# Performance work log

Measured on AMD Instinct MI355X. Metric: run time of the kernel, lower is better.

Reference implementation:

```python
import jax, jax.numpy as jnp
import numpy as np

D_MODEL = 1024
D_STATE = 16
D_CONV = 4
EXPAND = 2
DT_RANK = 64  # ceil(d_model / 16)
D_INNER = D_MODEL * EXPAND
BATCH, SEQ_LEN = 2, 2048


def setup_inputs() -> dict:
    key = jax.random.key(0)
    ks = jax.random.split(key, 6)
    s = lambda k, shape, scale: jax.random.normal(k, shape, dtype=jnp.float32) * scale
    x = jax.random.normal(ks[0], (BATCH, SEQ_LEN, D_MODEL), dtype=jnp.float32)
    in_proj_w = s(ks[1], (2 * D_INNER, D_MODEL), D_MODEL ** -0.5)
    conv_w = s(ks[2], (D_INNER, 1, D_CONV), D_CONV ** -0.5)  # depthwise kernel [O, I/groups=1, K]
    conv_b = jnp.zeros((D_INNER,), jnp.float32)
    # HiPPO-inspired init: A_log[d, n] = log(n+1)
    A_log = jnp.log(jnp.broadcast_to(jnp.arange(1, D_STATE + 1, dtype=jnp.float32), (D_INNER, D_STATE)))
    x_proj_w = s(ks[3], (DT_RANK + 2 * D_STATE, D_INNER), D_INNER ** -0.5)
    dt_proj_w = s(ks[4], (D_INNER, DT_RANK), DT_RANK ** -0.5)
    dt_proj_b = jnp.zeros((D_INNER,), jnp.float32)
    D_param = jnp.ones((D_INNER,), jnp.float32)
    out_proj_w = s(ks[5], (D_MODEL, D_INNER), D_INNER ** -0.5)
    return {"x": x, "in_proj_w": in_proj_w, "conv_w": conv_w, "conv_b": conv_b,
            "A_log": A_log, "x_proj_w": x_proj_w, "dt_proj_w": dt_proj_w,
            "dt_proj_b": dt_proj_b, "D": D_param, "out_proj_w": out_proj_w}


def reference(x, in_proj_w, conv_w, conv_b, A_log, x_proj_w, dt_proj_w, dt_proj_b, D, out_proj_w):
    B, L, _ = x.shape
    # input projection -> [B, L, 2*d_inner], split into ssm branch and gate
    xz = x @ in_proj_w.T
    xc, z = jnp.split(xz, 2, axis=-1)
    # depthwise causal conv1d: torch pads (d_conv-1) both sides then truncates -> left pad only
    xt = jnp.transpose(xc, (0, 2, 1))  # [B, d_inner, L]
    xt = jax.lax.conv_general_dilated(
        xt, conv_w, window_strides=(1,), padding=[(D_CONV - 1, 0)],
        dimension_numbers=("NCH", "OIH", "NCH"), feature_group_count=D_INNER)
    xt = xt + conv_b[None, :, None]
    xs = jnp.transpose(xt, (0, 2, 1))  # [B, L, d_inner]
    # input-dependent dt, B, C
    x_dbl = xs @ x_proj_w.T  # [B, L, dt_rank + 2*d_state]
    dt, Bm, Cm = jnp.split(x_dbl, [DT_RANK, DT_RANK + D_STATE], axis=-1)
    dt = jax.nn.softplus(dt @ dt_proj_w.T + dt_proj_b)  # [B, L, d_inner]
    A = -jnp.exp(A_log)  # [d_inner, d_state]

    def step(h, inp):
        x_t, dt_t, B_t, C_t = inp  # [B,d_inner], [B,d_inner], [B,d_state], [B,d_state]
        dA = jnp.exp(dt_t[..., None] * A)                       # [B, d_inner, d_state]
        h = dA * h + (dt_t * x_t)[..., None] * B_t[:, None, :]  # [B, d_inner, d_state]
        y = jnp.einsum("bds,bs->bd", h, C_t)
        return h, y

    h0 = jnp.zeros((B, D_INNER, D_STATE), dtype=x.dtype)
    _, ys = jax.lax.scan(step, h0, (jnp.transpose(xs, (1, 0, 2)),
                                    jnp.transpose(dt, (1, 0, 2)),
                                    jnp.transpose(Bm, (1, 0, 2)),
                                    jnp.transpose(Cm, (1, 0, 2))))
    y = jnp.transpose(ys, (1, 0, 2)) + D * xs          # skip term D * x
    y = y * (z * jax.nn.sigmoid(z))                    # SiLU gate
    return y @ out_proj_w.T
```

## Files before the change

### kernel.cpp

```cpp
#include <hip/hip_runtime.h>
#include <cstdint>
#include <cmath>

#define BATCH   2
#define SEQ     2048
#define DMODEL  1024
#define DINNER  2048
#define DSTATE  16
#define DTRANK  64
#define BL      (BATCH*SEQ)
#define LOG2E   1.44269504088896340736f

typedef __bf16 bf16_t;
typedef bf16_t bf16x4 __attribute__((ext_vector_type(4)));
typedef bf16_t bf16x8 __attribute__((ext_vector_type(8)));
typedef float  f32x4  __attribute__((ext_vector_type(4)));

#define SWZ(r, g) ((g) ^ (((r) >> 1) & 3))

__device__ __forceinline__ void gl16(const bf16_t* g, bf16_t* lds) {
  __builtin_amdgcn_global_load_lds((const __attribute__((address_space(1))) void*)g,
                                   (__attribute__((address_space(3))) void*)lds, 16, 0, 0);
}

__global__ __launch_bounds__(256)
void gemm_hl_mfma(const bf16_t* __restrict__ Ah, const bf16_t* __restrict__ Al,
                  const bf16_t* __restrict__ Wh, const bf16_t* __restrict__ Wl,
                  float* __restrict__ C, int K, int lda, int ldw, int ldc) {
  __shared__ bf16_t smem[2][16384];
  const int m0  = blockIdx.y * 128;
  const int n0  = blockIdx.x * 128;
  const int tid = threadIdx.x;
  const int l   = tid & 63;
  const int w   = tid >> 6;
  const int wr  = w >> 1, wc = w & 1;

  const int r1 = tid >> 2, r2 = (256 + tid) >> 2;
  const int g1 = SWZ(r1, tid & 3), g2 = SWZ(r2, tid & 3);
  const int lb1 = w * 512, lb2 = 2048 + w * 512;
  const int fr = l & 15, kg = l >> 4;

  const size_t kbase = (size_t)blockIdx.z * K;
  C += (size_t)blockIdx.z * (size_t)gridDim.y * 128 * ldc;

  const size_t a1b = (size_t)(m0 + r1) * lda + kbase + g1 * 8;
  const size_t a2b = (size_t)(m0 + r2) * lda + kbase + g2 * 8;
  const size_t w1b = (size_t)(n0 + r1) * ldw + kbase + g1 * 8;
  const size_t w2b = (size_t)(n0 + r2) * ldw + kbase + g2 * 8;

  f32x4 acc[4][4];
#pragma unroll
  for (int i = 0; i < 4; ++i)
#pragma unroll
    for (int j = 0; j < 4; ++j)
      acc[i][j] = (f32x4){0.f, 0.f, 0.f, 0.f};

  const int NT = K >> 5;
  {
    bf16_t* sb = smem[0];
    gl16(Ah + a1b, sb + lb1);         gl16(Ah + a2b, sb + lb2);
    gl16(Al + a1b, sb + 4096 + lb1);  gl16(Al + a2b, sb + 4096 + lb2);
    gl16(Wh + w1b, sb + 8192 + lb1);  gl16(Wh + w2b, sb + 8192 + lb2);
    gl16(Wl + w1b, sb + 12288 + lb1); gl16(Wl + w2b, sb + 12288 + lb2);
  }
  asm volatile("s_waitcnt vmcnt(0)" ::: "memory");
  __syncthreads();

  for (int kt = 0; kt < NT; ++kt) {
    bf16_t* sb = smem[kt & 1];
    if (kt + 1 < NT) {
      bf16_t* sn = smem[(kt + 1) & 1];
      const size_t ko = (size_t)(kt + 1) << 5;
      gl16(Ah + a1b + ko, sn + lb1);         gl16(Ah + a2b + ko, sn + lb2);
      gl16(Al + a1b + ko, sn + 4096 + lb1);  gl16(Al + a2b + ko, sn + 4096 + lb2);
      gl16(Wh + w1b + ko, sn + 8192 + lb1);  gl16(Wh + w2b + ko, sn + 8192 + lb2);
      gl16(Wl + w1b + ko, sn + 12288 + lb1); gl16(Wl + w2b + ko, sn + 12288 + lb2);
    }
    bf16x8 ah[4], al[4], bh[4], bl[4];
#pragma unroll
    for (int mi = 0; mi < 4; ++mi) {
      const int R = wr * 64 + mi * 16 + fr;
      const int e = R * 32 + SWZ(R, kg) * 8;
      ah[mi] = *reinterpret_cast<const bf16x8*>(&sb[e]);
      al[mi] = *reinterpret_cast<const bf16x8*>(&sb[4096 + e]);
    }
#pragma unroll
    for (int ni = 0; ni < 4; ++ni) {
      const int R = wc * 64 + ni * 16 + fr;
      const int e = R * 32 + SWZ(R, kg) * 8;
      bh[ni] = *reinterpret_cast<const bf16x8*>(&sb[8192 + e]);
      bl[ni] = *reinterpret_cast<const bf16x8*>(&sb[12288 + e]);
    }
#pragma unroll
    for (int mi = 0; mi < 4; ++mi)
#pragma unroll
      for (int ni = 0; ni < 4; ++ni) {
        acc[mi][ni] = __builtin_amdgcn_mfma_f32_16x16x32_bf16(ah[mi], bh[ni], acc[mi][ni], 0, 0, 0);
        acc[mi][ni] = __builtin_amdgcn_mfma_f32_16x16x32_bf16(ah[mi], bl[ni], acc[mi][ni], 0, 0, 0);
        acc[mi][ni] = __builtin_amdgcn_mfma_f32_16x16x32_bf16(al[mi], bh[ni], acc[mi][ni], 0, 0, 0);
      }
    if (kt + 1 < NT) asm volatile("s_waitcnt vmcnt(0)" ::: "memory");
    __syncthreads();
  }

#pragma unroll
  for (int mi = 0; mi < 4; ++mi)
#pragma unroll
    for (int i = 0; i < 4; ++i) {
      const int row = m0 + wr * 64 + mi * 16 + (l >> 4) * 4 + i;
#pragma unroll
      for (int ni = 0; ni < 4; ++ni)
        C[(size_t)row * ldc + n0 + wc * 64 + ni * 16 + (l & 15)] = acc[mi][ni][i];
    }
}

__device__ __forceinline__ void cvt4_store(float4 v, bf16_t* hi, bf16_t* lo, int i) {
  bf16x4 h, lv;
  h[0] = (bf16_t)v.x; h[1] = (bf16_t)v.y; h[2] = (bf16_t)v.z; h[3] = (bf16_t)v.w;
  lv[0] = (bf16_t)(v.x - (float)h[0]); lv[1] = (bf16_t)(v.y - (float)h[1]);
  lv[2] = (bf16_t)(v.z - (float)h[2]); lv[3] = (bf16_t)(v.w - (float)h[3]);
  reinterpret_cast<bf16x4*>(hi)[i] = h;
  reinterpret_cast<bf16x4*>(lo)[i] = lv;
}

#define Q1 1048576
#define Q2 (Q1 + 1048576)
#define Q3 (Q2 + 524288)
#define Q4 (Q3 + 32768)
#define Q5 (Q4 + 65536)

__global__ __launch_bounds__(256)
void prep(const float* __restrict__ x, const float* __restrict__ inw,
          const float* __restrict__ outw, const float* __restrict__ dtw,
          const float* __restrict__ xprojw,
          bf16_t* xhi, bf16_t* xlo, bf16_t* iwhi, bf16_t* iwlo,
          bf16_t* owh, bf16_t* owl, bf16_t* dtwh, bf16_t* dtwl,
          bf16_t* xpwh, bf16_t* xpwl) {
  const int i = blockIdx.x * 256 + threadIdx.x;
  if (i < Q1) {
    cvt4_store(reinterpret_cast<const float4*>(x)[i], xhi, xlo, i);
  } else if (i < Q2) {
    const int j = i - Q1;
    cvt4_store(reinterpret_cast<const float4*>(inw)[j], iwhi, iwlo, j);
  } else if (i < Q3) {
    const int j = i - Q2;
    cvt4_store(reinterpret_cast<const float4*>(outw)[j], owh, owl, j);
  } else if (i < Q4) {
    const int j = i - Q3;
    cvt4_store(reinterpret_cast<const float4*>(dtw)[j], dtwh, dtwl, j);
  } else if (i < Q5) {
    const int j = i - Q4;
    const int row = j >> 9;
    float4 v = make_float4(0.f, 0.f, 0.f, 0.f);
    if (row < 96) v = reinterpret_cast<const float4*>(xprojw)[j];
    cvt4_store(v, xpwh, xpwl, j);
  }
}

__global__ __launch_bounds__(256)
void reduce_xdbl(const float* __restrict__ part, float* __restrict__ xdbl,
                 bf16_t* __restrict__ xdh, bf16_t* __restrict__ xdl) {
  const int i = blockIdx.x * 256 + threadIdx.x;
  float4 s = reinterpret_cast<const float4*>(part)[i];
#pragma unroll
  for (int p = 1; p < 8; ++p) {
    const float4 v = reinterpret_cast<const float4*>(part)[(size_t)p * 131072 + i];
    s.x += v.x; s.y += v.y; s.z += v.z; s.w += v.w;
  }
  reinterpret_cast<float4*>(xdbl)[i] = s;
  cvt4_store(s, xdh, xdl, i);
}

__global__ __launch_bounds__(256)
void conv1d_causal_hl(const float* __restrict__ xz, const float* __restrict__ cw,
                      const float* __restrict__ cb, bf16_t* __restrict__ xshi,
                      bf16_t* __restrict__ xslo) {
  const int idx = blockIdx.x * 256 + threadIdx.x;
  const int dq  = idx & 511;
  const int bl  = idx >> 9;
  const int lpos = bl & (SEQ - 1);
  const int d   = dq * 4;

  float wv[4][4];
#pragma unroll
  for (int j = 0; j < 4; ++j)
#pragma unroll
    for (int k = 0; k < 4; ++k)
      wv[j][k] = cw[(size_t)(d + j) * 4 + k];

  float4 acc = *reinterpret_cast<const float4*>(&cb[d]);
#pragma unroll
  for (int k = 0; k < 4; ++k) {
    const int ls = lpos - 3 + k;
    if (ls >= 0) {
      const float4 v = *reinterpret_cast<const float4*>(&xz[(size_t)(bl - 3 + k) * 4096 + d]);
      acc.x += v.x * wv[0][k];
      acc.y += v.y * wv[1][k];
      acc.z += v.z * wv[2][k];
      acc.w += v.w * wv[3][k];
    }
  }
  bf16x4 h, lv;
  h[0] = (bf16_t)acc.x; h[1] = (bf16_t)acc.y; h[2] = (bf16_t)acc.z; h[3] = (bf16_t)acc.w;
  lv[0] = (bf16_t)(acc.x - (float)h[0]); lv[1] = (bf16_t)(acc.y - (float)h[1]);
  lv[2] = (bf16_t)(acc.z - (float)h[2]); lv[3] = (bf16_t)(acc.w - (float)h[3]);
  *reinterpret_cast<bf16x4*>(&xshi[(size_t)bl * 2048 + d]) = h;
  *reinterpret_cast<bf16x4*>(&xslo[(size_t)bl * 2048 + d]) = lv;
}

__device__ __forceinline__ float softplus_f(float v) {
  return fmaxf(v, 0.0f) + log1pf(expf(-fabsf(v)));
}
__device__ __forceinline__ float silu_f(float v) {
  return v / (1.0f + expf(-v));
}

__global__ __launch_bounds__(256)
void scan_pass1(const float* __restrict__ dtg, const bf16_t* __restrict__ xshi,
                const bf16_t* __restrict__ xslo, const float* __restrict__ xdbl,
                const float* __restrict__ alog, const float* __restrict__ dtb,
                float* __restrict__ hP, int NC, int Lc) {
  const int tid = threadIdx.x;
  const int d = blockIdx.x * 256 + tid;
  const int c = blockIdx.y;
  const int b = blockIdx.z;
  __shared__ float sB[64][16];

  float A2[16];
#pragma unroll
  for (int q = 0; q < 4; ++q) {
    const float4 v = *reinterpret_cast<const float4*>(&alog[(size_t)d * 16 + q * 4]);
    A2[q*4+0] = -expf(v.x) * LOG2E; A2[q*4+1] = -expf(v.y) * LOG2E;
    A2[q*4+2] = -expf(v.z) * LOG2E; A2[q*4+3] = -expf(v.w) * LOG2E;
  }
  const float dtbd = dtb[d];

  float h[16];
#pragma unroll
  for (int n = 0; n < 16; ++n) h[n] = 0.f;
  float S = 0.f;

  const int row0c = b * SEQ + c * Lc;
  for (int t0 = 0; t0 < Lc; t0 += 64) {
    const int rows = min(64, Lc - t0);
    __syncthreads();
    for (int j = tid; j < rows * 4; j += 256) {
      const int r = j >> 2, q = j & 3;
      *reinterpret_cast<float4*>(&sB[r][q*4]) =
        *reinterpret_cast<const float4*>(&xdbl[(size_t)(row0c + t0 + r) * 128 + 64 + q*4]);
    }
    __syncthreads();
#pragma unroll 2
    for (int t = 0; t < rows; ++t) {
      const size_t row = (size_t)(row0c + t0 + t);
      const float dtr = dtg[row * 2048 + d];
      const float xv  = (float)xshi[row * 2048 + d] + (float)xslo[row * 2048 + d];
      const float dt  = softplus_f(dtr + dtbd);
      S += dt;
      const float dtx = dt * xv;
#pragma unroll
      for (int n = 0; n < 16; ++n)
        h[n] = fmaf(exp2f(dt * A2[n]), h[n], dtx * sB[t][n]);
    }
  }
  const size_t o = ((((size_t)b * 2048 + d) * NC) + c) * 32;
#pragma unroll
  for (int n = 0; n < 16; ++n) {
    hP[o + n]      = h[n];
    hP[o + 16 + n] = exp2f(A2[n] * S);
  }
}

__global__ __launch_bounds__(256)
void scan_pass2(float* __restrict__ hP, int NC) {
  const int lane = threadIdx.x & 63;
  const int bd   = blockIdx.x * 4 + (threadIdx.x >> 6);
  const int c    = lane < NC ? lane : NC - 1;
  const size_t base = ((size_t)bd * NC + c) * 32;

  float h[16], P[16];
#pragma unroll
  for (int q = 0; q < 4; ++q) {
    const float4 v = *reinterpret_cast<const float4*>(&hP[base + q * 4]);
    h[q*4]=v.x; h[q*4+1]=v.y; h[q*4+2]=v.z; h[q*4+3]=v.w;
    const float4 p = *reinterpret_cast<const float4*>(&hP[base + 16 + q * 4]);
    P[q*4]=p.x; P[q*4+1]=p.y; P[q*4+2]=p.z; P[q*4+3]=p.w;
  }

#pragma unroll
  for (int s = 1; s < 64; s <<= 1) {
    float hf[16], Pf[16];
#pragma unroll
    for (int n = 0; n < 16; ++n) { hf[n] = __shfl_up(h[n], s, 64); Pf[n] = __shfl_up(P[n], s, 64); }
    if (lane >= s) {
#pragma unroll
      for (int n = 0; n < 16; ++n) { h[n] = fmaf(P[n], hf[n], h[n]); P[n] *= Pf[n]; }
    }
  }
  float hx[16];
#pragma unroll
  for (int n = 0; n < 16; ++n) {
    hx[n] = __shfl_up(h[n], 1, 64);
    if (lane == 0) hx[n] = 0.f;
  }
  if (lane < NC) {
#pragma unroll
    for (int q = 0; q < 4; ++q)
      *reinterpret_cast<float4*>(&hP[base + q * 4]) =
        make_float4(hx[q*4], hx[q*4+1], hx[q*4+2], hx[q*4+3]);
  }
}

__global__ __launch_bounds__(256)
void scan_pass3(const float* __restrict__ dtg, const bf16_t* __restrict__ xshi,
                const bf16_t* __restrict__ xslo, const float* __restrict__ xdbl,
                const float* __restrict__ xz, const float* __restrict__ alog,
                const float* __restrict__ dtb, const float* __restrict__ Dp,
                const float* __restrict__ hP, bf16_t* __restrict__ ghi,
                bf16_t* __restrict__ glo, int NC, int Lc) {
  const int tid = threadIdx.x;
  const int d = blockIdx.x * 256 + tid;
  const int c = blockIdx.y;
  const int b = blockIdx.z;
  __shared__ float sB[64][16];
  __shared__ float sC[64][16];

  float A2[16];
#pragma unroll
  for (int q = 0; q < 4; ++q) {
    const float4 v = *reinterpret_cast<const float4*>(&alog[(size_t)d * 16 + q * 4]);
    A2[q*4+0] = -expf(v.x) * LOG2E; A2[q*4+1] = -expf(v.y) * LOG2E;
    A2[q*4+2] = -expf(v.z) * LOG2E; A2[q*4+3] = -expf(v.w) * LOG2E;
  }
  const float dtbd = dtb[d];
  const float Dv   = Dp[d];

  float h[16];
  const size_t o = ((((size_t)b * 2048 + d) * NC) + c) * 32;
#pragma unroll
  for (int q = 0; q < 4; ++q) {
    const float4 v = *reinterpret_cast<const float4*>(&hP[o + q * 4]);
    h[q*4]=v.x; h[q*4+1]=v.y; h[q*4+2]=v.z; h[q*4+3]=v.w;
  }

  const int row0c = b * SEQ + c * Lc;
  for (int t0 = 0; t0 < Lc; t0 += 64) {
    const int rows = min(64, Lc - t0);
    __syncthreads();
    for (int j = tid; j < rows * 8; j += 256) {
      const int r = j >> 3, q = j & 7;
      const float4 v =
        *reinterpret_cast<const float4*>(&xdbl[(size_t)(row0c + t0 + r) * 128 + 64 + q*4]);
      if (q < 4) *reinterpret_cast<float4*>(&sB[r][q*4])     = v;
      else       *reinterpret_cast<float4*>(&sC[r][(q-4)*4]) = v;
    }
    __syncthreads();
#pragma unroll 2
    for (int t = 0; t < rows; ++t) {
      const size_t row = (size_t)(row0c + t0 + t);
      const float dtr = dtg[row * 2048 + d];
      const float xv  = (float)xshi[row * 2048 + d] + (float)xslo[row * 2048 + d];
      const float zv  = xz [row * 4096 + 2048 + d];
      const float dt  = softplus_f(dtr + dtbd);
      const float dtx = dt * xv;
      float ya[4] = {0.f, 0.f, 0.f, 0.f};
#pragma unroll
      for (int n = 0; n < 16; ++n) {
        h[n] = fmaf(exp2f(dt * A2[n]), h[n], dtx * sB[t][n]);
        ya[n & 3] = fmaf(h[n], sC[t][n], ya[n & 3]);
      }
      const float y = (ya[0] + ya[1]) + (ya[2] + ya[3]);
      const float gv = (y + Dv * xv) * silu_f(zv);
      const bf16_t gh = (bf16_t)gv;
      ghi[row * 2048 + d] = gh;
      glo[row * 2048 + d] = (bf16_t)(gv - (float)gh);
    }
  }
}

extern "C" void kernel_launch(void* const* d_in, const int* in_sizes, int n_in,
                              void* d_out, int out_size, void* d_ws, size_t ws_size,
                              hipStream_t stream) {
  const float* x      = (const float*)d_in[0];
  const float* inw    = (const float*)d_in[1];
  const float* convw  = (const float*)d_in[2];
  const float* convb  = (const float*)d_in[3];
  const float* alog   = (const float*)d_in[4];
  const float* xprojw = (const float*)d_in[5];
  const float* dtw    = (const float*)d_in[6];
  const float* dtb    = (const float*)d_in[7];
  const float* Dp     = (const float*)d_in[8];
  const float* outw   = (const float*)d_in[9];
  float* out = (float*)d_out;

  char* p = (char*)d_ws;
  float* xz    = (float*)p;  p += (size_t)BL * 4096 * 4;
  float* xdbl  = (float*)p;  p += (size_t)BL * 128 * 4;
  float* dtg   = (float*)p;  p += (size_t)BL * 2048 * 4;
  bf16_t* xhi  = (bf16_t*)p; p += (size_t)BL * 1024 * 2;
  bf16_t* xlo  = (bf16_t*)p; p += (size_t)BL * 1024 * 2;
  bf16_t* iwhi = (bf16_t*)p; p += (size_t)DINNER*2*1024*2;
  bf16_t* iwlo = (bf16_t*)p; p += (size_t)DINNER*2*1024*2;
  bf16_t* xshi = (bf16_t*)p; p += (size_t)BL * 2048 * 2;
  bf16_t* xslo = (bf16_t*)p; p += (size_t)BL * 2048 * 2;
  bf16_t* xpwh = (bf16_t*)p; p += (size_t)128 * 2048 * 2;
  bf16_t* xpwl = (bf16_t*)p; p += (size_t)128 * 2048 * 2;
  bf16_t* xdh  = (bf16_t*)p; p += (size_t)BL * 128 * 2;
  bf16_t* xdl  = (bf16_t*)p; p += (size_t)BL * 128 * 2;
  bf16_t* dtwh = (bf16_t*)p; p += (size_t)2048 * 64 * 2;
  bf16_t* dtwl = (bf16_t*)p; p += (size_t)2048 * 64 * 2;
  bf16_t* owh  = (bf16_t*)p; p += (size_t)1024 * 2048 * 2;
  bf16_t* owl  = (bf16_t*)p; p += (size_t)1024 * 2048 * 2;
  float* hP    = (float*)p;
  float* xpart = (float*)xhi;
  bf16_t* ghi  = xhi;
  bf16_t* glo  = xhi + (size_t)BL * 2048;

  const size_t base_bytes = (size_t)(p - (char*)d_ws);
  int NC = 64;
  while (NC > 1 && base_bytes + (size_t)BATCH * 2048 * NC * 32 * 4 > ws_size)
    NC >>= 1;
  const int Lc = SEQ / NC;

  prep<<<(Q5 + 255) / 256, 256, 0, stream>>>(x, inw, outw, dtw, xprojw,
      xhi, xlo, iwhi, iwlo, owh, owl, dtwh, dtwl, xpwh, xpwl);
  gemm_hl_mfma<<<dim3(32, 32, 1), 256, 0, stream>>>(xhi, xlo, iwhi, iwlo, xz,
                                                    1024, 1024, 1024, 4096);
  conv1d_causal_hl<<<8192, 256, 0, stream>>>(xz, convw, convb, xshi, xslo);
  gemm_hl_mfma<<<dim3(1, 32, 8), 256, 0, stream>>>(xshi, xslo, xpwh, xpwl, xpart,
                                                   256, 2048, 2048, 128);
  reduce_xdbl<<<512, 256, 0, stream>>>(xpart, xdbl, xdh, xdl);
  gemm_hl_mfma<<<dim3(16, 32, 1), 256, 0, stream>>>(xdh, xdl, dtwh, dtwl, dtg,
                                                    64, 128, 64, 2048);
  scan_pass1<<<dim3(8, NC, 2), 256, 0, stream>>>(dtg, xshi, xslo, xdbl, alog, dtb, hP, NC, Lc);
  scan_pass2<<<1024, 256, 0, stream>>>(hP, NC);
  scan_pass3<<<dim3(8, NC, 2), 256, 0, stream>>>(dtg, xshi, xslo, xdbl, xz, alog, dtb,
                                                 Dp, hP, ghi, glo, NC, Lc);
  gemm_hl_mfma<<<dim3(8, 32, 1), 256, 0, stream>>>(ghi, glo, owh, owl, out,
                                                   2048, 2048, 2048, 1024);
}
```

Before: 517.4 us.

## Fuse softplus and SiLU into GEMM epilogues and use hardware exp2/log2/rcp

Moves the dt softplus (with bias) into the dt-projection GEMM epilogue and the z SiLU into the in-projection GEMM epilogue, so both scan passes read precomputed values. The scan passes stop recomputing softplus twice per element. All exponentials in the scan recurrence now use raw v_exp_f32 instead of exp2f. This removes transcendental work from the serial scan loops, at the cost of slightly lower accuracy from the hardware approximations, and the xz buffer now holds silu(z) rather than z.

```diff
diff --git a/kernel.cpp b/kernel.cpp
--- a/kernel.cpp
+++ b/kernel.cpp
@@ -23,10 +23,22 @@
                                    (__attribute__((address_space(3))) void*)lds, 16, 0, 0);
 }
 
+__device__ __forceinline__ float exp2_hw(float x) { float r; asm("v_exp_f32 %0, %1" : "=v"(r) : "v"(x)); return r; }
+__device__ __forceinline__ float log2_hw(float x) { float r; asm("v_log_f32 %0, %1" : "=v"(r) : "v"(x)); return r; }
+__device__ __forceinline__ float rcp_hw(float x)  { float r; asm("v_rcp_f32 %0, %1" : "=v"(r) : "v"(x)); return r; }
+
+__device__ __forceinline__ float silu_fast(float v) {
+  return v * rcp_hw(1.0f + exp2_hw(-v * LOG2E));
+}
+__device__ __forceinline__ float softplus_fast(float v) {
+  return fmaxf(v, 0.0f) + log2_hw(1.0f + exp2_hw(-fabsf(v) * LOG2E)) * (1.0f / LOG2E);
+}
+
 __global__ __launch_bounds__(256)
 void gemm_hl_mfma(const bf16_t* __restrict__ Ah, const bf16_t* __restrict__ Al,
                   const bf16_t* __restrict__ Wh, const bf16_t* __restrict__ Wl,
-                  float* __restrict__ C, int K, int lda, int ldw, int ldc) {
+                  float* __restrict__ C, int K, int lda, int ldw, int ldc,
+                  const float* __restrict__ bias, int epi) {
   __shared__ bf16_t smem[2][16384];
   const int m0  = blockIdx.y * 128;
   const int n0  = blockIdx.x * 128;
@@ -104,14 +116,22 @@
   }
 
 #pragma unroll
-  for (int mi = 0; mi < 4; ++mi)
-#pragma unroll
-    for (int i = 0; i < 4; ++i) {
-      const int row = m0 + wr * 64 + mi * 16 + (l >> 4) * 4 + i;
-#pragma unroll
-      for (int ni = 0; ni < 4; ++ni)
-        C[(size_t)row * ldc + n0 + wc * 64 + ni * 16 + (l & 15)] = acc[mi][ni][i];
-    }
+  for (int ni = 0; ni < 4; ++ni) {
+    const int col = n0 + wc * 64 + ni * 16 + (l & 15);
+    float bcol = 0.f;
+    if (epi == 1) bcol = bias[col];
+    const bool dosilu = (epi == 2) && (col >= 2048);
+#pragma unroll
+    for (int mi = 0; mi < 4; ++mi)
+#pragma unroll
+      for (int i = 0; i < 4; ++i) {
+        const int row = m0 + wr * 64 + mi * 16 + (l >> 4) * 4 + i;
+        float v = acc[mi][ni][i];
+        if (epi == 1)      v = softplus_fast(v + bcol);
+        else if (dosilu)   v = silu_fast(v);
+        C[(size_t)row * ldc + col] = v;
+      }
+  }
 }
 
 __device__ __forceinline__ void cvt4_store(float4 v, bf16_t* hi, bf16_t* lo, int i) {
@@ -208,18 +228,11 @@
   *reinterpret_cast<bf16x4*>(&xslo[(size_t)bl * 2048 + d]) = lv;
 }
 
-__device__ __forceinline__ float softplus_f(float v) {
-  return fmaxf(v, 0.0f) + log1pf(expf(-fabsf(v)));
-}
-__device__ __forceinline__ float silu_f(float v) {
-  return v / (1.0f + expf(-v));
-}
-
-__global__ __launch_bounds__(256)
-void scan_pass1(const float* __restrict__ dtg, const bf16_t* __restrict__ xshi,
+__global__ __launch_bounds__(256)
+void scan_pass1(const float* __restrict__ dtv, const bf16_t* __restrict__ xshi,
                 const bf16_t* __restrict__ xslo, const float* __restrict__ xdbl,
-                const float* __restrict__ alog, const float* __restrict__ dtb,
-                float* __restrict__ hP, int NC, int Lc) {
+                const float* __restrict__ alog, float* __restrict__ hP,
+                int NC, int Lc) {
   const int tid = threadIdx.x;
   const int d = blockIdx.x * 256 + tid;
   const int c = blockIdx.y;
@@ -230,10 +243,9 @@
 #pragma unroll
   for (int q = 0; q < 4; ++q) {
     const float4 v = *reinterpret_cast<const float4*>(&alog[(size_t)d * 16 + q * 4]);
-    A2[q*4+0] = -expf(v.x) * LOG2E; A2[q*4+1] = -expf(v.y) * LOG2E;
-    A2[q*4+2] = -expf(v.z) * LOG2E; A2[q*4+3] = -expf(v.w) * LOG2E;
-  }
-  const float dtbd = dtb[d];
+    A2[q*4+0] = -exp2_hw(v.x * LOG2E) * LOG2E; A2[q*4+1] = -exp2_hw(v.y * LOG2E) * LOG2E;
+    A2[q*4+2] = -exp2_hw(v.z * LOG2E) * LOG2E; A2[q*4+3] = -exp2_hw(v.w * LOG2E) * LOG2E;
+  }
 
   float h[16];
 #pragma unroll
@@ -253,21 +265,20 @@
 #pragma unroll 2
     for (int t = 0; t < rows; ++t) {
       const size_t row = (size_t)(row0c + t0 + t);
-      const float dtr = dtg[row * 2048 + d];
-      const float xv  = (float)xshi[row * 2048 + d] + (float)xslo[row * 2048 + d];
-      const float dt  = softplus_f(dtr + dtbd);
+      const float dt = dtv[row * 2048 + d];
+      const float xv = (float)xshi[row * 2048 + d] + (float)xslo[row * 2048 + d];
       S += dt;
       const float dtx = dt * xv;
 #pragma unroll
       for (int n = 0; n < 16; ++n)
-        h[n] = fmaf(exp2f(dt * A2[n]), h[n], dtx * sB[t][n]);
+        h[n] = fmaf(exp2_hw(dt * A2[n]), h[n], dtx * sB[t][n]);
     }
   }
   const size_t o = ((((size_t)b * 2048 + d) * NC) + c) * 32;
 #pragma unroll
   for (int n = 0; n < 16; ++n) {
     hP[o + n]      = h[n];
-    hP[o + 16 + n] = exp2f(A2[n] * S);
+    hP[o + 16 + n] = exp2_hw(A2[n] * S);
   }
 }
 
@@ -312,12 +323,12 @@
 }
 
 __global__ __launch_bounds__(256)
-void scan_pass3(const float* __restrict__ dtg, const bf16_t* __restrict__ xshi,
+void scan_pass3(const float* __restrict__ dtv, const bf16_t* __restrict__ xshi,
                 const bf16_t* __restrict__ xslo, const float* __restrict__ xdbl,
                 const float* __restrict__ xz, const float* __restrict__ alog,
-                const float* __restrict__ dtb, const float* __restrict__ Dp,
-                const float* __restrict__ hP, bf16_t* __restrict__ ghi,
-                bf16_t* __restrict__ glo, int NC, int Lc) {
+                const float* __restrict__ Dp, const float* __restrict__ hP,
+                bf16_t* __restrict__ ghi, bf16_t* __restrict__ glo,
+                int NC, int Lc) {
   const int tid = threadIdx.x;
   const int d = blockIdx.x * 256 + tid;
   const int c = blockIdx.y;
@@ -329,11 +340,10 @@
 #pragma unroll
   for (int q = 0; q < 4; ++q) {
     const float4 v = *reinterpret_cast<const float4*>(&alog[(size_t)d * 16 + q * 4]);
-    A2[q*4+0] = -expf(v.x) * LOG2E; A2[q*4+1] = -expf(v.y) * LOG2E;
-    A2[q*4+2] = -expf(v.z) * LOG2E; A2[q*4+3] = -expf(v.w) * LOG2E;
-  }
-  const float dtbd = dtb[d];
-  const float Dv   = Dp[d];
+    A2[q*4+0] = -exp2_hw(v.x * LOG2E) * LOG2E; A2[q*4+1] = -exp2_hw(v.y * LOG2E) * LOG2E;
+    A2[q*4+2] = -exp2_hw(v.z * LOG2E) * LOG2E; A2[q*4+3] = -exp2_hw(v.w * LOG2E) * LOG2E;
+  }
+  const float Dv = Dp[d];
 
   float h[16];
   const size_t o = ((((size_t)b * 2048 + d) * NC) + c) * 32;
@@ -358,19 +368,18 @@
 #pragma unroll 2
     for (int t = 0; t < rows; ++t) {
       const size_t row = (size_t)(row0c + t0 + t);
-      const float dtr = dtg[row * 2048 + d];
-      const float xv  = (float)xshi[row * 2048 + d] + (float)xslo[row * 2048 + d];
-      const float zv  = xz [row * 4096 + 2048 + d];
-      const float dt  = softplus_f(dtr + dtbd);
+      const float dt = dtv[row * 2048 + d];
+      const float xv = (float)xshi[row * 2048 + d] + (float)xslo[row * 2048 + d];
+      const float zs = xz [row * 4096 + 2048 + d];
       const float dtx = dt * xv;
       float ya[4] = {0.f, 0.f, 0.f, 0.f};
 #pragma unroll
       for (int n = 0; n < 16; ++n) {
-        h[n] = fmaf(exp2f(dt * A2[n]), h[n], dtx * sB[t][n]);
+        h[n] = fmaf(exp2_hw(dt * A2[n]), h[n], dtx * sB[t][n]);
         ya[n & 3] = fmaf(h[n], sC[t][n], ya[n & 3]);
       }
       const float y = (ya[0] + ya[1]) + (ya[2] + ya[3]);
-      const float gv = (y + Dv * xv) * silu_f(zv);
+      const float gv = (y + Dv * xv) * zs;
       const bf16_t gh = (bf16_t)gv;
       ghi[row * 2048 + d] = gh;
       glo[row * 2048 + d] = (bf16_t)(gv - (float)gh);
@@ -425,17 +434,17 @@
   prep<<<(Q5 + 255) / 256, 256, 0, stream>>>(x, inw, outw, dtw, xprojw,
       xhi, xlo, iwhi, iwlo, owh, owl, dtwh, dtwl, xpwh, xpwl);
   gemm_hl_mfma<<<dim3(32, 32, 1), 256, 0, stream>>>(xhi, xlo, iwhi, iwlo, xz,
-                                                    1024, 1024, 1024, 4096);
+                                                    1024, 1024, 1024, 4096, nullptr, 2);
   conv1d_causal_hl<<<8192, 256, 0, stream>>>(xz, convw, convb, xshi, xslo);
   gemm_hl_mfma<<<dim3(1, 32, 8), 256, 0, stream>>>(xshi, xslo, xpwh, xpwl, xpart,
-                                                   256, 2048, 2048, 128);
+                                                   256, 2048, 2048, 128, nullptr, 0);
   reduce_xdbl<<<512, 256, 0, stream>>>(xpart, xdbl, xdh, xdl);
   gemm_hl_mfma<<<dim3(16, 32, 1), 256, 0, stream>>>(xdh, xdl, dtwh, dtwl, dtg,
-                                                    64, 128, 64, 2048);
-  scan_pass1<<<dim3(8, NC, 2), 256, 0, stream>>>(dtg, xshi, xslo, xdbl, alog, dtb, hP, NC, Lc);
+                                                    64, 128, 64, 2048, dtb, 1);
+  scan_pass1<<<dim3(8, NC, 2), 256, 0, stream>>>(dtg, xshi, xslo, xdbl, alog, hP, NC, Lc);
   scan_pass2<<<1024, 256, 0, stream>>>(hP, NC);
-  scan_pass3<<<dim3(8, NC, 2), 256, 0, stream>>>(dtg, xshi, xslo, xdbl, xz, alog, dtb,
+  scan_pass3<<<dim3(8, NC, 2), 256, 0, stream>>>(dtg, xshi, xslo, xdbl, xz, alog,
                                                  Dp, hP, ghi, glo, NC, Lc);
   gemm_hl_mfma<<<dim3(8, 32, 1), 256, 0, stream>>>(ghi, glo, owh, owl, out,
-                                                   2048, 2048, 2048, 1024);
-}
+                                                   2048, 2048, 2048, 1024, nullptr, 0);
+}
```

New measurement: 431.8 us. 16.5% less time.
